# Optimization experiments

Hardware: AMD Instinct MI355X
Metric: run time of the kernel (lower is better)

The kernel has to match this reference:

```python
import jax, jax.numpy as jnp
import numpy as np

OFFS = [(0, 0), (1, 0), (-1, 0), (0, 1), (0, -1), (1, -1), (-1, 1)]  # (dq, dr)
B, H, W, E, NH, L = 16, 64, 64, 254, 8, 8
C = E + 2          # d_model = 256
DFF = 4 * C        # 1024
MLP = 512
VOCAB = 9


def setup_inputs():
    ks = jax.random.split(jax.random.key(0), 24)
    r = lambda k, s: jax.random.normal(k, s, dtype=jnp.float32) * 0.05
    return {
        'grid': jax.random.randint(ks[0], (B, H, W), 0, VOCAB),
        'gold': jax.random.normal(ks[1], (B, 2), dtype=jnp.float32),
        'emb': r(ks[2], (VOCAB, E)),
        'in_w': r(ks[3], (L, 3 * C, C)), 'in_b': r(ks[4], (L, 3 * C)),
        'out_w': r(ks[5], (L, C, C)), 'out_b': r(ks[6], (L, C)),
        'l1_w': r(ks[7], (L, DFF, C)), 'l1_b': r(ks[8], (L, DFF)),
        'l2_w': r(ks[9], (L, C, DFF)), 'l2_b': r(ks[10], (L, C)),
        'n1_g': jnp.ones((L, C)), 'n1_b': jnp.zeros((L, C)),
        'n2_g': jnp.ones((L, C)), 'n2_b': jnp.zeros((L, C)),
        'fn_g': jnp.ones((C,)), 'fn_b': jnp.zeros((C,)),
        'pw1': r(ks[11], (MLP, C)), 'pb1': r(ks[12], (MLP,)),
        'pw2': r(ks[13], (3, MLP)), 'pb2': r(ks[14], (3,)),
        'cw1': r(ks[15], (128, C)), 'cb1': r(ks[16], (128,)),
        'cw2': r(ks[17], (1, 128)), 'cb2': r(ks[18], (1,)),
    }


def _ln(x, g, b, eps=1e-5):
    m = jnp.mean(x, -1, keepdims=True)
    v = jnp.mean(jnp.square(x - m), -1, keepdims=True)
    return (x - m) * jax.lax.rsqrt(v + eps) * g + b


def _hex_gather(x):
    # x: (B,H,W,C) -> (B,H,W,7,C); out-of-bounds neighbors are zero vectors
    b, h, w, c = x.shape
    xp = jnp.pad(x, ((0, 0), (1, 1), (1, 1), (0, 0)))
    feats = [xp[:, 1 + dr:1 + dr + h, 1 + dq:1 + dq + w, :] for (dq, dr) in OFFS]
    return jnp.stack(feats, axis=3)


def _mha(x, kv, w_in, b_in, w_out, b_out):
    # x: (B,H,W,C) queries; kv: (B,H,W,7,C); full-bias projections, no mask
    c = x.shape[-1]
    hd = c // NH
    wq, wk, wv = w_in[:c], w_in[c:2 * c], w_in[2 * c:]
    bq, bk, bv = b_in[:c], b_in[c:2 * c], b_in[2 * c:]
    q = (x @ wq.T + bq).reshape(*x.shape[:-1], NH, hd)
    k = (kv @ wk.T + bk).reshape(*kv.shape[:-1], NH, hd)
    v = (kv @ wv.T + bv).reshape(*kv.shape[:-1], NH, hd)
    scores = jnp.einsum('bxyne,bxykne->bxynk', q, k) / np.sqrt(hd).astype(np.float32)
    attn = jax.nn.softmax(scores, axis=-1)
    o = jnp.einsum('bxynk,bxykne->bxyne', attn, v)
    o = o.reshape(*x.shape[:-1], c)
    return o @ w_out.T + b_out


def _pos_embed(h, w, d):
    half = d // 2
    div = jnp.exp(jnp.arange(0, half, 2, dtype=jnp.float32) * (-np.log(10000.0) / half))
    pw = jnp.arange(w, dtype=jnp.float32)[:, None] * div
    pe_w = jnp.concatenate([jnp.sin(pw), jnp.cos(pw)], -1)  # (W, 2*len(div))
    ph = jnp.arange(h, dtype=jnp.float32)[:, None] * div
    pe_h = jnp.concatenate([jnp.sin(ph), jnp.cos(ph)], -1)
    cw, ch = pe_w.shape[-1], pe_h.shape[-1]
    pe = jnp.zeros((h, w, d), dtype=jnp.float32)
    pe = pe.at[:, :, :cw].set(jnp.broadcast_to(pe_w[None, :, :], (h, w, cw)))
    pe = pe.at[:, :, cw:cw + ch].set(jnp.broadcast_to(pe_h[:, None, :], (h, w, ch)))
    return pe


def _forward(grid, gold, emb, in_w, in_b, out_w, out_b, l1_w, l1_b, l2_w, l2_b,
             n1_g, n1_b, n2_g, n2_b, fn_g, fn_b, pw1, pb1, pw2, pb2, cw1, cb1, cw2, cb2):
    b, h, w = grid.shape
    feats = jnp.concatenate(
        [emb[grid], jnp.broadcast_to(gold[:, None, None, :], (b, h, w, 2))], -1)
    x = feats + _pos_embed(h, w, C)[None]
    for i in range(L):
        kvg = _hex_gather(x)
        a = _mha(x, kvg, in_w[i], in_b[i], out_w[i], out_b[i])
        x = _ln(x + a, n1_g[i], n1_b[i])
        ff = jax.nn.relu(x @ l1_w[i].T + l1_b[i]) @ l2_w[i].T + l2_b[i]
        x = _ln(x + ff, n2_g[i], n2_b[i])
    x = _ln(x, fn_g, fn_b)
    pooled = jnp.mean(x, axis=(1, 2))  # (B,C) critic adaptive-avg-pool
    value = (jax.nn.relu(pooled @ cw1.T + cb1) @ cw2.T + cb2)[:, 0]
    pol = jax.nn.relu(x @ pw1.T + pb1) @ pw2.T + pb2  # (B,H,W,3)
    return pol[..., 2], pol[..., 0], pol[..., 1], value


def reference(grid, gold, emb, in_w, in_b, out_w, out_b, l1_w, l1_b, l2_w, l2_b,
              n1_g, n1_b, n2_g, n2_b, fn_g, fn_b, pw1, pb1, pw2, pb2, cw1, cb1, cw2, cb2):
    return _forward(grid, gold, emb, in_w, in_b, out_w, out_b, l1_w, l1_b, l2_w, l2_b,
                    n1_g, n1_b, n2_g, n2_b, fn_g, fn_b, pw1, pb1, pw2, pb2,
                    cw1, cb1, cw2, cb2)
```

## Files before the change

### kernel.cpp

```cpp
#include <hip/hip_runtime.h>

typedef __bf16 bf16x8 __attribute__((ext_vector_type(8)));
typedef float  f32x4  __attribute__((ext_vector_type(4)));
typedef unsigned short u16;
typedef u16 u16x8 __attribute__((ext_vector_type(8)));
typedef u16 u16x4 __attribute__((ext_vector_type(4)));

__device__ __forceinline__ float bf2f(u16 h) {
  union { unsigned u; float f; } w; w.u = ((unsigned)h) << 16; return w.f;
}
__device__ __forceinline__ u16 f2bf(float f) {
  union { float f; unsigned u; } w; w.f = f;
  return (u16)((w.u + 0x7fffu + ((w.u >> 16) & 1u)) >> 16);
}

__global__ __launch_bounds__(256)
void cvt_all(const float* __restrict__ s0, const float* __restrict__ s1,
             const float* __restrict__ s2, const float* __restrict__ s3,
             const float* __restrict__ s4, u16* __restrict__ dst) {
  long i = (long)blockIdx.x * 256 + threadIdx.x;
  float v;
  if (i < 1572864)      v = s0[i];
  else if (i < 2097152) v = s1[i - 1572864];
  else if (i < 4194304) v = s2[i - 2097152];
  else if (i < 6291456) v = s3[i - 4194304];
  else                  v = s4[i - 6291456];
  dst[i] = f2bf(v);
}

__global__ __launch_bounds__(256)
void embed_kernel(const int* __restrict__ grd, const float* __restrict__ gold,
                  const float* __restrict__ emb, u16* __restrict__ xbf) {
  int p = blockIdx.x, c = threadIdx.x;
  int y = p >> 6, xw = p & 63;
  int j = c & 63;
  float dv = expf(-(float)(2 * j) * (9.210340371976184f / 128.0f));
  float arg = ((c < 128) ? (float)xw : (float)y) * dv;
  float pos = (c & 64) ? cosf(arg) : sinf(arg);
  for (int b = 0; b < 16; ++b) {
    int t = b * 4096 + p;
    int g = grd[t];
    float v = (c < 254) ? emb[g * 254 + c] : gold[b * 2 + (c - 254)];
    xbf[(long)t * 256 + c] = f2bf(v + pos);
  }
}

template<int RELU, int ROWS>
__global__ __launch_bounds__(256)
void gemm_qn(const u16* __restrict__ A, const u16* __restrict__ W,
             const float* __restrict__ bias, u16* __restrict__ out,
             int Nout, int NT) {
  constexpr int NI = ROWS / 32;
  __shared__ u16 sA[ROWS * 256];
  __shared__ u16 sW[128 * 64];
  int tid = threadIdx.x;
  int lane = tid & 63, wave = tid >> 6;
  int wr = wave >> 1, wc = wave & 1;
  long rowbase = (long)blockIdx.x * ROWS;
  unsigned lbase = (unsigned)(tid & ~63) * 16;

  {
    int ac = tid & 31;
#pragma unroll
    for (int p = 0; p < ROWS / 8; ++p) {
      int row = p * 8 + (tid >> 5);
      int sc = (ac & 24) | ((ac ^ row) & 7);
      const u16* src = A + (rowbase + row) * 256 + sc * 8;
      __builtin_amdgcn_global_load_lds(
          (const __attribute__((address_space(1))) void*)src,
          (__attribute__((address_space(3))) void*)((char*)sA + p * 4096 + lbase),
          16, 0, 0);
    }
  }

  f32x4 acc[NI][4] = {};
  int T = NT * 4;
  for (int t = 0; t < T; ++t) {
    int nt = t >> 2, kc = t & 3;
    __syncthreads();
#pragma unroll
    for (int p = 0; p < 4; ++p) {
      int row = p * 32 + (tid >> 3);
      int sc = ((tid & 7) ^ row) & 7;
      const u16* src = W + (long)(nt * 128 + row) * 256 + kc * 64 + sc * 8;
      __builtin_amdgcn_global_load_lds(
          (const __attribute__((address_space(1))) void*)src,
          (__attribute__((address_space(3))) void*)((char*)sW + p * 4096 + lbase),
          16, 0, 0);
    }
    __syncthreads();

#pragma unroll
    for (int kk = 0; kk < 2; ++kk) {
      bf16x8 af[NI], bw[4];
#pragma unroll
      for (int i = 0; i < NI; ++i) {
        int ra = wr * (ROWS / 2) + i * 16 + (lane & 15);
        int l = kc * 8 + kk * 4 + (lane >> 4);
        int phys = (l & 24) | ((l ^ ra) & 7);
        af[i] = *(const bf16x8*)((const char*)sA + ra * 512 + phys * 16);
      }
#pragma unroll
      for (int j = 0; j < 4; ++j) {
        int rb = wc * 64 + j * 16 + (lane & 15);
        int m = kk * 4 + (lane >> 4);
        int phys = (m ^ rb) & 7;
        bw[j] = *(const bf16x8*)((const char*)sW + rb * 128 + phys * 16);
      }
#pragma unroll
      for (int i = 0; i < NI; ++i)
#pragma unroll
        for (int j = 0; j < 4; ++j)
          acc[i][j] = __builtin_amdgcn_mfma_f32_16x16x32_bf16(af[i], bw[j], acc[i][j], 0, 0, 0);
    }

    if (kc == 3) {
#pragma unroll
      for (int i = 0; i < NI; ++i) {
        long r0 = rowbase + wr * (ROWS / 2) + i * 16 + ((lane >> 4) * 4);
#pragma unroll
        for (int j = 0; j < 4; ++j) {
          long col = (long)nt * 128 + wc * 64 + j * 16 + (lane & 15);
          float bv = bias[col];
#pragma unroll
          for (int r = 0; r < 4; ++r) {
            float v = acc[i][j][r] + bv;
            if (RELU) v = fmaxf(v, 0.0f);
            out[(r0 + r) * Nout + col] = f2bf(v);
            acc[i][j][r] = 0.0f;
          }
        }
      }
    }
  }
}

__global__ __launch_bounds__(256)
void gemm_pol(const u16* __restrict__ A, const u16* __restrict__ W,
              const float* __restrict__ b1, const float* __restrict__ pw2,
              const float* __restrict__ pb2, float* __restrict__ out) {
  __shared__ u16 sA[64 * 256];
  __shared__ u16 sW[128 * 64];
  __shared__ float part[2][3][64];
  int tid = threadIdx.x;
  int lane = tid & 63, wave = tid >> 6;
  int wr = wave >> 1, wc = wave & 1;
  long rowbase = (long)blockIdx.x * 64;
  unsigned lbase = (unsigned)(tid & ~63) * 16;

  for (int i = tid; i < 384; i += 256) ((float*)part)[i] = 0.0f;

  {
    int ac = tid & 31;
#pragma unroll
    for (int p = 0; p < 8; ++p) {
      int row = p * 8 + (tid >> 5);
      int sc = (ac & 24) | ((ac ^ row) & 7);
      const u16* src = A + (rowbase + row) * 256 + sc * 8;
      __builtin_amdgcn_global_load_lds(
          (const __attribute__((address_space(1))) void*)src,
          (__attribute__((address_space(3))) void*)((char*)sA + p * 4096 + lbase),
          16, 0, 0);
    }
  }

  f32x4 acc[2][4] = {};
  for (int t = 0; t < 16; ++t) {
    int nt = t >> 2, kc = t & 3;
    __syncthreads();
#pragma unroll
    for (int p = 0; p < 4; ++p) {
      int row = p * 32 + (tid >> 3);
      int sc = ((tid & 7) ^ row) & 7;
      const u16* src = W + (long)(nt * 128 + row) * 256 + kc * 64 + sc * 8;
      __builtin_amdgcn_global_load_lds(
          (const __attribute__((address_space(1))) void*)src,
          (__attribute__((address_space(3))) void*)((char*)sW + p * 4096 + lbase),
          16, 0, 0);
    }
    __syncthreads();

#pragma unroll
    for (int kk = 0; kk < 2; ++kk) {
      bf16x8 af[2], bw[4];
#pragma unroll
      for (int i = 0; i < 2; ++i) {
        int ra = wr * 32 + i * 16 + (lane & 15);
        int l = kc * 8 + kk * 4 + (lane >> 4);
        int phys = (l & 24) | ((l ^ ra) & 7);
        af[i] = *(const bf16x8*)((const char*)sA + ra * 512 + phys * 16);
      }
#pragma unroll
      for (int j = 0; j < 4; ++j) {
        int rb = wc * 64 + j * 16 + (lane & 15);
        int m = kk * 4 + (lane >> 4);
        int phys = (m ^ rb) & 7;
        bw[j] = *(const bf16x8*)((const char*)sW + rb * 128 + phys * 16);
      }
#pragma unroll
      for (int i = 0; i < 2; ++i)
#pragma unroll
        for (int j = 0; j < 4; ++j)
          acc[i][j] = __builtin_amdgcn_mfma_f32_16x16x32_bf16(af[i], bw[j], acc[i][j], 0, 0, 0);
    }

    if (kc == 3) {
#pragma unroll
      for (int i = 0; i < 2; ++i) {
#pragma unroll
        for (int r = 0; r < 4; ++r) {
          float p0 = 0.f, p1 = 0.f, p2 = 0.f;
#pragma unroll
          for (int j = 0; j < 4; ++j) {
            int col = nt * 128 + wc * 64 + j * 16 + (lane & 15);
            float v = fmaxf(acc[i][j][r] + b1[col], 0.0f);
            p0 += v * pw2[col];
            p1 += v * pw2[512 + col];
            p2 += v * pw2[1024 + col];
            acc[i][j][r] = 0.0f;
          }
#pragma unroll
          for (int m = 1; m < 16; m <<= 1) {
            p0 += __shfl_xor(p0, m); p1 += __shfl_xor(p1, m); p2 += __shfl_xor(p2, m);
          }
          if ((lane & 15) == 0) {
            int row = wr * 32 + i * 16 + (lane >> 4) * 4 + r;
            part[wc][0][row] += p0;
            part[wc][1][row] += p1;
            part[wc][2][row] += p2;
          }
        }
      }
    }
  }

  __syncthreads();
  if (tid < 64) {
    long t = rowbase + tid;
    float a0 = part[0][0][tid] + part[1][0][tid];
    float a1 = part[0][1][tid] + part[1][1][tid];
    float a2 = part[0][2][tid] + part[1][2][tid];
    out[t]          = a2 + pb2[2];
    out[65536 + t]  = a0 + pb2[0];
    out[131072 + t] = a1 + pb2[1];
  }
}

template<int KC>
__global__ __launch_bounds__(256)
void gemm_rln(const u16* __restrict__ A, int lda, const u16* __restrict__ W,
              const float* __restrict__ bias, u16* __restrict__ xbf,
              const float* __restrict__ g, const float* __restrict__ b) {
  __shared__ __align__(16) char smem[40960];
  u16* sAr = (u16*)smem;
  u16* sWr = (u16*)(smem + 8192);
  float* red = (float*)smem;
  int tid = threadIdx.x;
  int lane = tid & 63, wave = tid >> 6;
  long rowbase = (long)blockIdx.x * 64;
  unsigned lbase = (unsigned)(tid & ~63) * 16;

  f32x4 acc[4][4] = {};
  for (int kc = 0; kc < KC; ++kc) {
    __syncthreads();
#pragma unroll
    for (int p = 0; p < 2; ++p) {
      int row = p * 32 + (tid >> 3);
      int sc = ((tid & 7) ^ row) & 7;
      const u16* src = A + (rowbase + row) * lda + kc * 64 + sc * 8;
      __builtin_amdgcn_global_load_lds(
          (const __attribute__((address_space(1))) void*)src,
          (__attribute__((address_space(3))) void*)((char*)sAr + p * 4096 + lbase),
          16, 0, 0);
    }
#pragma unroll
    for (int p = 0; p < 8; ++p) {
      int row = p * 32 + (tid >> 3);
      int sc = ((tid & 7) ^ row) & 7;
      const u16* src = W + (long)row * (KC * 64) + kc * 64 + sc * 8;
      __builtin_amdgcn_global_load_lds(
          (const __attribute__((address_space(1))) void*)src,
          (__attribute__((address_space(3))) void*)((char*)sWr + p * 4096 + lbase),
          16, 0, 0);
    }
    __syncthreads();

#pragma unroll
    for (int kk = 0; kk < 2; ++kk) {
      bf16x8 af[4], bw[4];
#pragma unroll
      for (int i = 0; i < 4; ++i) {
        int ra = i * 16 + (lane & 15);
        int m = kk * 4 + (lane >> 4);
        int phys = (m ^ ra) & 7;
        af[i] = *(const bf16x8*)((const char*)sAr + ra * 128 + phys * 16);
      }
#pragma unroll
      for (int j = 0; j < 4; ++j) {
        int rb = wave * 64 + j * 16 + (lane & 15);
        int m = kk * 4 + (lane >> 4);
        int phys = (m ^ rb) & 7;
        bw[j] = *(const bf16x8*)((const char*)sWr + rb * 128 + phys * 16);
      }
#pragma unroll
      for (int i = 0; i < 4; ++i)
#pragma unroll
        for (int j = 0; j < 4; ++j)
          acc[i][j] = __builtin_amdgcn_mfma_f32_16x16x32_bf16(af[i], bw[j], acc[i][j], 0, 0, 0);
    }
  }

  float gcol[4], bcol[4];
  long colb = wave * 64 + (lane & 15);
#pragma unroll
  for (int j = 0; j < 4; ++j) { gcol[j] = g[colb + j * 16]; bcol[j] = b[colb + j * 16]; }

  __syncthreads();

#pragma unroll
  for (int i = 0; i < 4; ++i) {
#pragma unroll
    for (int r = 0; r < 4; ++r) {
      int rowl = i * 16 + (lane >> 4) * 4 + r;
      long rbase = (rowbase + rowl) * 256;
      float ps = 0.f, pss = 0.f;
#pragma unroll
      for (int j = 0; j < 4; ++j) {
        float v = acc[i][j][r] + bias[colb + j * 16] + bf2f(xbf[rbase + colb + j * 16]);
        acc[i][j][r] = v;
        ps += v; pss += v * v;
      }
#pragma unroll
      for (int m = 1; m < 16; m <<= 1) { ps += __shfl_xor(ps, m); pss += __shfl_xor(pss, m); }
      if ((lane & 15) == 0) {
        red[wave * 64 + rowl] = ps;
        red[256 + wave * 64 + rowl] = pss;
      }
    }
  }
  __syncthreads();
  if (tid < 64) {
    float s = red[tid] + red[64 + tid] + red[128 + tid] + red[192 + tid];
    float ss = red[256 + tid] + red[320 + tid] + red[384 + tid] + red[448 + tid];
    float mean = s * (1.0f / 256.0f);
    float var = ss * (1.0f / 256.0f) - mean * mean;
    red[512 + tid * 2] = mean;
    red[512 + tid * 2 + 1] = rsqrtf(var + 1e-5f);
  }
  __syncthreads();

#pragma unroll
  for (int i = 0; i < 4; ++i) {
#pragma unroll
    for (int r = 0; r < 4; ++r) {
      int rowl = i * 16 + (lane >> 4) * 4 + r;
      float mean = red[512 + rowl * 2];
      float rstd = red[512 + rowl * 2 + 1];
      long rbase = (rowbase + rowl) * 256;
#pragma unroll
      for (int j = 0; j < 4; ++j) {
        float o = (acc[i][j][r] - mean) * rstd * gcol[j] + bcol[j];
        xbf[rbase + colb + j * 16] = f2bf(o);
      }
    }
  }
}

__global__ __launch_bounds__(256)
void attn_kernel(u16* __restrict__ qkv, const float* __restrict__ bin) {
  const int drA[7] = {0, 0, 0, 1, -1, -1, 1};
  const int dqA[7] = {0, 1, -1, 0, 0, 1, -1};
  int bid = blockIdx.x;
  int bswz = (bid & 7) * 512 + (bid >> 3);
  int gid = bswz * 256 + threadIdx.x;
  int t = gid >> 4;
  int sub = gid & 15;
  int hoff = sub * 16;
  int b = t >> 12, y = (t >> 6) & 63, xw = t & 63;
  long tbase = (long)t * 768 + hoff;

  long tn[7]; float okf[7];
#pragma unroll
  for (int n = 0; n < 7; ++n) {
    int yy = y + drA[n], xx = xw + dqA[n];
    bool ok = ((unsigned)yy < 64u) && ((unsigned)xx < 64u);
    int yc = yy < 0 ? 0 : (yy > 63 ? 63 : yy);
    int xc = xx < 0 ? 0 : (xx > 63 ? 63 : xx);
    tn[n] = ((long)(b * 4096 + yc * 64 + xc)) * 768 + hoff;
    okf[n] = ok ? 1.0f : 0.0f;
  }

  u16x8 qraw[2], kr[7][2];
  {
    const u16x8* qp = (const u16x8*)(qkv + tbase);
    qraw[0] = qp[0]; qraw[1] = qp[1];
  }
#pragma unroll
  for (int n = 0; n < 7; ++n) {
    const u16x8* kp = (const u16x8*)(qkv + tn[n] + 256);
    kr[n][0] = kp[0]; kr[n][1] = kp[1];
  }

  float q[16];
#pragma unroll
  for (int j = 0; j < 2; ++j)
#pragma unroll
    for (int e = 0; e < 8; ++e) q[j * 8 + e] = bf2f(qraw[j][e]);

  float skb = 0.f;
  {
    const float* kb = bin + 256 + hoff;
#pragma unroll
    for (int i = 0; i < 16; ++i) skb += q[i] * kb[i];
  }

  float s[7];
#pragma unroll
  for (int n = 0; n < 7; ++n) {
    float acc = 0.f;
#pragma unroll
    for (int j = 0; j < 2; ++j)
#pragma unroll
      for (int e = 0; e < 8; ++e) acc += q[j * 8 + e] * bf2f(kr[n][j][e]);
    float p = (okf[n] != 0.f) ? acc : skb;
    p += __shfl_xor(p, 1);
    s[n] = p * 0.17677669529663687f;
  }

  u16x8 vr[7][2];
#pragma unroll
  for (int n = 0; n < 7; ++n) {
    const u16x8* vp = (const u16x8*)(qkv + tn[n] + 512);
    vr[n][0] = vp[0]; vr[n][1] = vp[1];
  }

  float mx = s[0];
#pragma unroll
  for (int n = 1; n < 7; ++n) mx = fmaxf(mx, s[n]);
  float wsum = 0.0f;
#pragma unroll
  for (int n = 0; n < 7; ++n) { s[n] = expf(s[n] - mx); wsum += s[n]; }
  float inv = 1.0f / wsum;

  float o[16];
#pragma unroll
  for (int i = 0; i < 16; ++i) o[i] = 0.0f;
  float woob = 0.f;
#pragma unroll
  for (int n = 0; n < 7; ++n) {
    float wk = okf[n] * s[n];
    woob += s[n] - wk;
#pragma unroll
    for (int j = 0; j < 2; ++j)
#pragma unroll
      for (int e = 0; e < 8; ++e) o[j * 8 + e] += wk * bf2f(vr[n][j][e]);
  }
  {
    const float* vb = bin + 512 + hoff;
#pragma unroll
    for (int i = 0; i < 16; ++i) o[i] += woob * vb[i];
  }

  u16x8* op = (u16x8*)(qkv + tbase);
#pragma unroll
  for (int j = 0; j < 2; ++j) {
    u16x8 ov;
#pragma unroll
    for (int e = 0; e < 8; ++e) ov[e] = f2bf(o[j * 8 + e] * inv);
    op[j] = ov;
  }
}

__global__ __launch_bounds__(256)
void ln_kernel(u16* __restrict__ xbf, const float* __restrict__ g,
               const float* __restrict__ b) {
  int wave = threadIdx.x >> 6, lane = threadIdx.x & 63;
  long t = (long)blockIdx.x * 4 + wave;
  long base = t * 256 + lane * 4;
  u16x4 raw = *(const u16x4*)(xbf + base);
  float v0 = bf2f(raw[0]), v1 = bf2f(raw[1]), v2 = bf2f(raw[2]), v3 = bf2f(raw[3]);
  float s = v0 + v1 + v2 + v3;
  float ss = v0 * v0 + v1 * v1 + v2 * v2 + v3 * v3;
#pragma unroll
  for (int m = 1; m < 64; m <<= 1) { s += __shfl_xor(s, m); ss += __shfl_xor(ss, m); }
  float mean = s * (1.0f / 256.0f);
  float var = ss * (1.0f / 256.0f) - mean * mean;
  float rstd = rsqrtf(var + 1e-5f);
  float4 gv = *(const float4*)(g + lane * 4);
  float4 bv = *(const float4*)(b + lane * 4);
  u16x4 ob;
  ob[0] = f2bf((v0 - mean) * rstd * gv.x + bv.x);
  ob[1] = f2bf((v1 - mean) * rstd * gv.y + bv.y);
  ob[2] = f2bf((v2 - mean) * rstd * gv.z + bv.z);
  ob[3] = f2bf((v3 - mean) * rstd * gv.w + bv.w);
  *(u16x4*)(xbf + base) = ob;
}

__global__ __launch_bounds__(256)
void pool1_kernel(const u16* __restrict__ xbf, float* __restrict__ part) {
  int bid = blockIdx.x, c = threadIdx.x;
  long base = (long)bid * 128 * 256;
  float s = 0.f;
  for (int p = 0; p < 128; ++p) s += bf2f(xbf[base + (long)p * 256 + c]);
  part[(long)bid * 256 + c] = s;
}

__global__ __launch_bounds__(256)
void value_kernel(const float* __restrict__ part, const float* __restrict__ cw1,
                  const float* __restrict__ cb1, const float* __restrict__ cw2,
                  const float* __restrict__ cb2, float* __restrict__ out) {
  __shared__ float pooled[256];
  __shared__ float red[2];
  int b = blockIdx.x, c = threadIdx.x;
  float s = 0.f;
  for (int seg = 0; seg < 32; ++seg) s += part[((long)b * 32 + seg) * 256 + c];
  pooled[c] = s * (1.0f / 4096.0f);
  __syncthreads();
  if (c < 128) {
    float hj = cb1[c];
    const float* wr = cw1 + c * 256;
    for (int k = 0; k < 256; ++k) hj += pooled[k] * wr[k];
    hj = fmaxf(hj, 0.0f);
    float acc = hj * cw2[c];
#pragma unroll
    for (int m = 1; m < 64; m <<= 1) acc += __shfl_xor(acc, m);
    if ((c & 63) == 0) red[c >> 6] = acc;
  }
  __syncthreads();
  if (c == 0) out[196608 + b] = red[0] + red[1] + cb2[0];
}

extern "C" void kernel_launch(void* const* d_in, const int* in_sizes, int n_in,
                              void* d_out, int out_size, void* d_ws, size_t ws_size,
                              hipStream_t stream) {
  const int*   grd  = (const int*)d_in[0];
  const float* gold = (const float*)d_in[1];
  const float* emb  = (const float*)d_in[2];
  const float* in_w = (const float*)d_in[3];
  const float* in_b = (const float*)d_in[4];
  const float* out_w= (const float*)d_in[5];
  const float* out_b= (const float*)d_in[6];
  const float* l1_w = (const float*)d_in[7];
  const float* l1_b = (const float*)d_in[8];
  const float* l2_w = (const float*)d_in[9];
  const float* l2_b = (const float*)d_in[10];
  const float* n1_g = (const float*)d_in[11];
  const float* n1_b = (const float*)d_in[12];
  const float* n2_g = (const float*)d_in[13];
  const float* n2_b = (const float*)d_in[14];
  const float* fn_g = (const float*)d_in[15];
  const float* fn_b = (const float*)d_in[16];
  const float* pw1  = (const float*)d_in[17];
  const float* pb1  = (const float*)d_in[18];
  const float* pw2  = (const float*)d_in[19];
  const float* pb2  = (const float*)d_in[20];
  const float* cw1  = (const float*)d_in[21];
  const float* cb1  = (const float*)d_in[22];
  const float* cw2  = (const float*)d_in[23];
  const float* cb2  = (const float*)d_in[24];
  float* out = (float*)d_out;

  char* ws = (char*)d_ws;
  u16*   xbf    = (u16*)ws;
  char*  region = ws + (32l << 20);
  u16*   qkv    = (u16*)region;
  u16*   hbuf   = (u16*)region;
  u16*   wbf    = (u16*)(ws + (160l << 20));
  float* part   = (float*)(ws + (173l << 20));

  u16* inw_bf  = wbf;
  u16* outw_bf = inw_bf + 1572864;
  u16* l1w_bf  = outw_bf + 524288;
  u16* l2w_bf  = l1w_bf + 2097152;
  u16* pw1_bf  = l2w_bf + 2097152;

  cvt_all<<<25088, 256, 0, stream>>>(in_w, out_w, l1_w, l2_w, pw1, wbf);

  embed_kernel<<<4096, 256, 0, stream>>>(grd, gold, emb, xbf);

  for (int i = 0; i < 8; ++i) {
    gemm_qn<0, 128><<<512, 256, 0, stream>>>(
        xbf, inw_bf + (long)i * 196608, in_b + i * 768, qkv, 768, 6);
    attn_kernel<<<4096, 256, 0, stream>>>(qkv, in_b + i * 768);
    gemm_rln<4><<<1024, 256, 0, stream>>>(
        qkv, 768, outw_bf + (long)i * 65536, out_b + i * 256, xbf,
        n1_g + i * 256, n1_b + i * 256);
    gemm_qn<1, 128><<<512, 256, 0, stream>>>(
        xbf, l1w_bf + (long)i * 262144, l1_b + i * 1024, hbuf, 1024, 8);
    gemm_rln<16><<<1024, 256, 0, stream>>>(
        hbuf, 1024, l2w_bf + (long)i * 262144, l2_b + i * 256, xbf,
        n2_g + i * 256, n2_b + i * 256);
  }

  ln_kernel<<<16384, 256, 0, stream>>>(xbf, fn_g, fn_b);

  gemm_pol<<<1024, 256, 0, stream>>>(xbf, pw1_bf, pb1, pw2, pb2, out);

  pool1_kernel<<<512, 256, 0, stream>>>(xbf, part);
  value_kernel<<<16, 256, 0, stream>>>(part, cw1, cb1, cw2, cb2, out);
}
```

Baseline: 1.909 ms.

## Double-buffer gemm_rln K tiles to overlap global-to-LDS loads with MFMA

Restructures the gemm_rln main loop so each K step covers 32 instead of 64 and uses two LDS buffers. The next tile is loaded straight into LDS while MFMAs run on the current one, with one barrier per iteration. The XOR swizzle changes to match the 64-byte row stride. The intent is to hide global load latency behind compute, at the cost of twice as many loop iterations and barriers. Each iteration also has less work to cover a load, and the prefetch has no explicit wait for its LDS-DMA to finish before the data is read.

```diff
diff --git a/kernel.cpp b/kernel.cpp
--- a/kernel.cpp
+++ b/kernel.cpp
@@ -252,70 +252,68 @@
               const float* __restrict__ bias, u16* __restrict__ xbf,
               const float* __restrict__ g, const float* __restrict__ b) {
   __shared__ __align__(16) char smem[40960];
-  u16* sAr = (u16*)smem;
-  u16* sWr = (u16*)(smem + 8192);
   float* red = (float*)smem;
   int tid = threadIdx.x;
   int lane = tid & 63, wave = tid >> 6;
+  int kg = lane >> 4;
   long rowbase = (long)blockIdx.x * 64;
-  unsigned lbase = (unsigned)(tid & ~63) * 16;
-
-  f32x4 acc[4][4] = {};
-  for (int kc = 0; kc < KC; ++kc) {
-    __syncthreads();
-#pragma unroll
-    for (int p = 0; p < 2; ++p) {
-      int row = p * 32 + (tid >> 3);
-      int sc = ((tid & 7) ^ row) & 7;
-      const u16* src = A + (rowbase + row) * lda + kc * 64 + sc * 8;
+  const int KW = KC * 64;
+
+  auto stage = [&](int t, int buf) {
+    {
+      int row = tid >> 2, c = tid & 3;
+      int sc = (c ^ (row >> 1)) & 3;
+      const u16* src = A + (rowbase + row) * lda + t * 32 + sc * 8;
       __builtin_amdgcn_global_load_lds(
           (const __attribute__((address_space(1))) void*)src,
-          (__attribute__((address_space(3))) void*)((char*)sAr + p * 4096 + lbase),
+          (__attribute__((address_space(3))) void*)(smem + buf * 4096 + tid * 16),
           16, 0, 0);
     }
 #pragma unroll
-    for (int p = 0; p < 8; ++p) {
-      int row = p * 32 + (tid >> 3);
-      int sc = ((tid & 7) ^ row) & 7;
-      const u16* src = W + (long)row * (KC * 64) + kc * 64 + sc * 8;
+    for (int p = 0; p < 4; ++p) {
+      int row = p * 64 + (tid >> 2), c = tid & 3;
+      int sc = (c ^ (row >> 1)) & 3;
+      const u16* src = W + (long)row * KW + t * 32 + sc * 8;
       __builtin_amdgcn_global_load_lds(
           (const __attribute__((address_space(1))) void*)src,
-          (__attribute__((address_space(3))) void*)((char*)sWr + p * 4096 + lbase),
+          (__attribute__((address_space(3))) void*)(smem + 8192 + buf * 16384 + p * 4096 + tid * 16),
           16, 0, 0);
     }
+  };
+
+  stage(0, 0);
+  __syncthreads();
+
+  f32x4 acc[4][4] = {};
+  const int NTI = KC * 2;
+  for (int t = 0; t < NTI; ++t) {
+    int cur = t & 1;
+    if (t + 1 < NTI) stage(t + 1, cur ^ 1);
+    bf16x8 af[4], bw[4];
+#pragma unroll
+    for (int i = 0; i < 4; ++i) {
+      int ra = i * 16 + (lane & 15);
+      int phys = (kg ^ (ra >> 1)) & 3;
+      af[i] = *(const bf16x8*)(smem + cur * 4096 + ra * 64 + phys * 16);
+    }
+#pragma unroll
+    for (int j = 0; j < 4; ++j) {
+      int rb = wave * 64 + j * 16 + (lane & 15);
+      int phys = (kg ^ (rb >> 1)) & 3;
+      bw[j] = *(const bf16x8*)(smem + 8192 + cur * 16384 + rb * 64 + phys * 16);
+    }
+#pragma unroll
+    for (int i = 0; i < 4; ++i)
+#pragma unroll
+      for (int j = 0; j < 4; ++j)
+        acc[i][j] = __builtin_amdgcn_mfma_f32_16x16x32_bf16(af[i], bw[j], acc[i][j], 0, 0, 0);
     __syncthreads();
-
-#pragma unroll
-    for (int kk = 0; kk < 2; ++kk) {
-      bf16x8 af[4], bw[4];
-#pragma unroll
-      for (int i = 0; i < 4; ++i) {
-        int ra = i * 16 + (lane & 15);
-        int m = kk * 4 + (lane >> 4);
-        int phys = (m ^ ra) & 7;
-        af[i] = *(const bf16x8*)((const char*)sAr + ra * 128 + phys * 16);
-      }
-#pragma unroll
-      for (int j = 0; j < 4; ++j) {
-        int rb = wave * 64 + j * 16 + (lane & 15);
-        int m = kk * 4 + (lane >> 4);
-        int phys = (m ^ rb) & 7;
-        bw[j] = *(const bf16x8*)((const char*)sWr + rb * 128 + phys * 16);
-      }
-#pragma unroll
-      for (int i = 0; i < 4; ++i)
-#pragma unroll
-        for (int j = 0; j < 4; ++j)
-          acc[i][j] = __builtin_amdgcn_mfma_f32_16x16x32_bf16(af[i], bw[j], acc[i][j], 0, 0, 0);
-    }
   }
 
   float gcol[4], bcol[4];
   long colb = wave * 64 + (lane & 15);
 #pragma unroll
   for (int j = 0; j < 4; ++j) { gcol[j] = g[colb + j * 16]; bcol[j] = b[colb + j * 16]; }
-
-  __syncthreads();
 
 #pragma unroll
   for (int i = 0; i < 4; ++i) {
```

Result: slower. 1.948 ms (+2.0%).
